# Performance work log

Hardware: AMD Instinct MI355X
Metric: run time of the kernel (lower is better)

## Reference

```python
import jax, jax.numpy as jnp
import numpy as np
from jax import lax

C = 64          # in_c
D_INNER = 128   # expand=2 * C
D_STATE = 16
D_CONV = 4
DT_RANK = 4     # ceil(C/16)
B, H, W = 4, 64, 64


def setup_inputs() -> dict:
    key = jax.random.key(0)
    ks = jax.random.split(key, 22)
    def n(k, shape, s=0.05):
        return jax.random.normal(k, shape, jnp.float32) * s
    inp = {}
    inp["x"] = jax.random.normal(ks[0], (B, C, H, W), jnp.float32)
    # AxialDW: depthwise (3,1) and (1,3) convs, groups=C
    inp["dwh_w"] = n(ks[1], (C, 1, 3, 1), 0.2); inp["dwh_b"] = n(ks[2], (C,))
    inp["dww_w"] = n(ks[3], (C, 1, 1, 3), 0.2); inp["dww_b"] = n(ks[4], (C,))
    # 1x1 conv
    inp["conv_w"] = n(ks[5], (C, C, 1, 1), 0.1); inp["conv_b"] = n(ks[6], (C,))
    # BatchNorm (eval mode, running stats)
    inp["bn_g"] = jnp.ones((C,), jnp.float32); inp["bn_b"] = jnp.zeros((C,), jnp.float32)
    inp["bn_m"] = n(ks[7], (C,), 0.1)
    inp["bn_v"] = jnp.abs(n(ks[8], (C,), 0.1)) + 1.0
    # ResMambaBlock: LayerNorm + Mamba(d_model=C) + residual
    inp["ln_g"] = jnp.ones((C,), jnp.float32); inp["ln_b"] = jnp.zeros((C,), jnp.float32)
    inp["in_proj_w"] = n(ks[9], (2 * D_INNER, C))
    inp["convd_w"] = n(ks[10], (D_INNER, 1, D_CONV), 0.2); inp["convd_b"] = n(ks[11], (D_INNER,))
    inp["x_proj_w"] = n(ks[12], (DT_RANK + 2 * D_STATE, D_INNER))
    inp["dt_proj_w"] = n(ks[13], (D_INNER, DT_RANK), 0.2)
    inp["dt_proj_b"] = n(ks[14], (D_INNER,), 0.5) - 4.0  # softplus -> small dt
    inp["A_log"] = jnp.log(jnp.tile(jnp.arange(1, D_STATE + 1, dtype=jnp.float32), (D_INNER, 1)))
    inp["Dp"] = jnp.ones((D_INNER,), jnp.float32)
    inp["out_proj_w"] = n(ks[15], (C, D_INNER))
    return inp


def _mamba(h, in_proj_w, convd_w, convd_b, x_proj_w, dt_proj_w, dt_proj_b, A_log, Dp, out_proj_w):
    # h: [B, L, C]
    Bt, L, _ = h.shape
    xz = jnp.einsum('blc,dc->bld', h, in_proj_w)          # [B,L,2*D_INNER]
    xm, z = jnp.split(xz, 2, axis=-1)
    # causal depthwise conv1d over L
    xc = lax.conv_general_dilated(xm.transpose(0, 2, 1), convd_w, (1,), [(D_CONV - 1, 0)],
                                  feature_group_count=D_INNER,
                                  dimension_numbers=('NCH', 'OIH', 'NCH'))
    xc = jax.nn.silu(xc + convd_b[None, :, None]).transpose(0, 2, 1)  # [B,L,D_INNER]
    dbc = jnp.einsum('bld,ed->ble', xc, x_proj_w)
    dt, Bm, Cm = jnp.split(dbc, [DT_RANK, DT_RANK + D_STATE], axis=-1)
    dt = jax.nn.softplus(jnp.einsum('blr,dr->bld', dt, dt_proj_w) + dt_proj_b)  # [B,L,D_INNER]
    A = -jnp.exp(A_log)                                    # [D_INNER, D_STATE]
    dA = jnp.exp(dt[..., None] * A)                        # [B,L,D_INNER,D_STATE]
    dBx = dt[..., None] * Bm[:, :, None, :] * xc[..., None]  # [B,L,D_INNER,D_STATE]

    def step(hc, inp):
        dA_t, dBx_t, C_t = inp
        hc = hc * dA_t + dBx_t                             # [B,D_INNER,D_STATE]
        y = jnp.einsum('bds,bs->bd', hc, C_t)
        return hc, y

    h0 = jnp.zeros((Bt, D_INNER, D_STATE), h.dtype)
    _, ys = lax.scan(step, h0, (dA.transpose(1, 0, 2, 3), dBx.transpose(1, 0, 2, 3), Cm.transpose(1, 0, 2)))
    ys = ys.transpose(1, 0, 2)                             # [B,L,D_INNER]
    ys = (ys + xc * Dp) * jax.nn.silu(z)
    return jnp.einsum('bld,cd->blc', ys, out_proj_w)


def _forward(x, dwh_w, dwh_b, dww_w, dww_b, conv_w, conv_b, bn_g, bn_b, bn_m, bn_v,
             ln_g, ln_b, in_proj_w, convd_w, convd_b, x_proj_w, dt_proj_w, dt_proj_b,
             A_log, Dp, out_proj_w):
    dn = ('NCHW', 'OIHW', 'NCHW')
    xh = lax.conv_general_dilated(x, dwh_w, (1, 1), 'SAME', feature_group_count=C, dimension_numbers=dn)
    xw = lax.conv_general_dilated(x, dww_w, (1, 1), 'SAME', feature_group_count=C, dimension_numbers=dn)
    x = x + xh + dwh_b[None, :, None, None] + xw + dww_b[None, :, None, None]
    x = lax.conv_general_dilated(x, conv_w, (1, 1), 'SAME', dimension_numbers=dn) + conv_b[None, :, None, None]
    x = (x - bn_m[None, :, None, None]) * lax.rsqrt(bn_v + 1e-5)[None, :, None, None] \
        * bn_g[None, :, None, None] + bn_b[None, :, None, None]
    x = jax.nn.relu(x)
    # ResMambaBlock: LN + Mamba + residual over tokens [B, H*W, C]
    Bt, Cc, Hh, Ww = x.shape
    seq = x.reshape(Bt, Cc, Hh * Ww).transpose(0, 2, 1)    # [B,L,C]
    mu = seq.mean(-1, keepdims=True)
    var = ((seq - mu) ** 2).mean(-1, keepdims=True)
    hn = (seq - mu) * lax.rsqrt(var + 1e-5) * ln_g + ln_b
    y = _mamba(hn, in_proj_w, convd_w, convd_b, x_proj_w, dt_proj_w, dt_proj_b, A_log, Dp, out_proj_w)
    out = (y + seq).transpose(0, 2, 1).reshape(Bt, Cc, Hh, Ww)
    return out


def reference(x, dwh_w, dwh_b, dww_w, dww_b, conv_w, conv_b, bn_g, bn_b, bn_m, bn_v,
              ln_g, ln_b, in_proj_w, convd_w, convd_b, x_proj_w, dt_proj_w, dt_proj_b,
              A_log, Dp, out_proj_w):
    return _forward(x, dwh_w, dwh_b, dww_w, dww_b, conv_w, conv_b, bn_g, bn_b, bn_m, bn_v,
                    ln_g, ln_b, in_proj_w, convd_w, convd_b, x_proj_w, dt_proj_w, dt_proj_b,
                    A_log, Dp, out_proj_w)
```

## Files before the change

### kernel.cpp

```cpp
#include <hip/hip_runtime.h>
#include <hip/hip_bf16.h>
#include <math.h>

#define BB 4
#define CC 64
#define LL 4096
#define DI 128
#define DS 16
#define NC 64
#define CL 64

__global__ __launch_bounds__(256) void k12_front(
    const float* __restrict__ x, const float* __restrict__ dwh_w,
    const float* __restrict__ dwh_b, const float* __restrict__ dww_w,
    const float* __restrict__ dww_b, const float* __restrict__ conv_w,
    const float* __restrict__ conv_b, const float* __restrict__ bn_g,
    const float* __restrict__ bn_b, const float* __restrict__ bn_m,
    const float* __restrict__ bn_v, const float* __restrict__ ln_g,
    const float* __restrict__ ln_b, float* __restrict__ seqT,
    float* __restrict__ hn) {
  __shared__ __align__(16) float tsm[64 * 68];
  __shared__ __align__(16) float wt[64 * 68];
  __shared__ float vsm[64 * 65];
  int tid = threadIdx.x;
  int blk = blockIdx.x;
  int b = blk >> 6, h = blk & 63;
  for (int i = tid; i < 4096; i += 256) {
    int co = i >> 6, ci = i & 63;
    wt[ci * 68 + co] = conv_w[i];
  }
  for (int i = tid; i < 4096; i += 256) {
    int c = i >> 6, w = i & 63;
    int base = ((b * 64 + c) << 12) + (h << 6) + w;
    float cen = x[base];
    float up = (h > 0)  ? x[base - 64] : 0.f;
    float dn = (h < 63) ? x[base + 64] : 0.f;
    float lf = (w > 0)  ? x[base - 1]  : 0.f;
    float rt = (w < 63) ? x[base + 1]  : 0.f;
    float t = cen + dwh_w[c*3]*up + dwh_w[c*3+1]*cen + dwh_w[c*3+2]*dn + dwh_b[c]
                  + dww_w[c*3]*lf + dww_w[c*3+1]*cen + dww_w[c*3+2]*rt + dww_b[c];
    tsm[c * 68 + w] = t;
  }
  __syncthreads();
  int co0 = (tid & 15) << 2;
  int w0  = (tid >> 4) << 2;
  float acc[4][4] = {};
  #pragma unroll 8
  for (int ci = 0; ci < 64; ++ci) {
    const float4 w4 = *(const float4*)&wt[ci * 68 + co0];
    const float4 t4 = *(const float4*)&tsm[ci * 68 + w0];
    const float wv[4] = {w4.x, w4.y, w4.z, w4.w};
    const float tv[4] = {t4.x, t4.y, t4.z, t4.w};
    #pragma unroll
    for (int jc = 0; jc < 4; ++jc)
      #pragma unroll
      for (int iw = 0; iw < 4; ++iw)
        acc[jc][iw] = fmaf(wv[jc], tv[iw], acc[jc][iw]);
  }
  #pragma unroll
  for (int j = 0; j < 4; ++j) {
    int co = co0 + j;
    float sc = bn_g[co] * rsqrtf(bn_v[co] + 1e-5f);
    float sh = bn_b[co] - bn_m[co] * sc;
    float cb = conv_b[co];
    float4 o4;
    float* oo = (float*)&o4;
    #pragma unroll
    for (int i = 0; i < 4; ++i) {
      float v = fmaxf(fmaf(acc[j][i] + cb, sc, sh), 0.f);
      vsm[(w0 + i) * 65 + co] = v;
      oo[i] = v;
    }
    *(float4*)&seqT[((size_t)(b * 64 + co) << 12) + (h << 6) + w0] = o4;
  }
  __syncthreads();
  int lane = tid & 63, wv_ = tid >> 6;
  float lg = ln_g[lane], lb = ln_b[lane];
  for (int k = 0; k < 16; ++k) {
    int w = wv_ * 16 + k;
    float v = vsm[w * 65 + lane];
    float sum = v, sq = v * v;
    #pragma unroll
    for (int off = 1; off < 64; off <<= 1) {
      sum += __shfl_xor(sum, off, 64);
      sq  += __shfl_xor(sq,  off, 64);
    }
    float mu  = sum * (1.f / 64.f);
    float var = sq * (1.f / 64.f) - mu * mu;
    float inv = rsqrtf(var + 1e-5f);
    hn[((size_t)((b << 12) + (h << 6) + w) << 6) + lane] = (v - mu) * inv * lg + lb;
  }
}

__global__ __launch_bounds__(256) void k3_inproj(
    const float* __restrict__ hn, const float* __restrict__ ipw,
    float* __restrict__ xm, float* __restrict__ z) {
  __shared__ __align__(16) float wsm[64 * 132];
  __shared__ __align__(16) float hsm[64 * 68];
  int tid = threadIdx.x;
  int half = blockIdx.y;
  int blk = blockIdx.x;
  int b  = blk >> 6;
  int l0 = (blk & 63) << 6;
  const float* wsrc = ipw + half * 8192;
  for (int i = tid; i < 8192; i += 256) {
    int d = i >> 6, c = i & 63;
    wsm[c * 132 + d] = wsrc[i];
  }
  for (int i = tid; i < 4096; i += 256) {
    int t = i >> 6, c = i & 63;
    hsm[c * 68 + t] = hn[((size_t)(b * LL + l0) << 6) + i];
  }
  __syncthreads();
  int d0 = (tid & 31) << 2;
  int t0 = (tid >> 5) << 3;
  float acc[4][8] = {};
  #pragma unroll 8
  for (int c = 0; c < 64; ++c) {
    const float4 w4 = *(const float4*)&wsm[c * 132 + d0];
    const float4 h0 = *(const float4*)&hsm[c * 68 + t0];
    const float4 h1 = *(const float4*)&hsm[c * 68 + t0 + 4];
    const float wv[4] = {w4.x, w4.y, w4.z, w4.w};
    const float hv[8] = {h0.x, h0.y, h0.z, h0.w, h1.x, h1.y, h1.z, h1.w};
    #pragma unroll
    for (int i = 0; i < 4; ++i)
      #pragma unroll
      for (int j = 0; j < 8; ++j)
        acc[i][j] = fmaf(wv[i], hv[j], acc[i][j]);
  }
  float* dst = half ? z : xm;
  #pragma unroll
  for (int j = 0; j < 8; ++j) {
    float4 v = make_float4(acc[0][j], acc[1][j], acc[2][j], acc[3][j]);
    *(float4*)&dst[((size_t)(b * LL + l0 + t0 + j) << 7) + d0] = v;
  }
}

__global__ __launch_bounds__(128) void k4_conv_proj(
    const float* __restrict__ xm, const float* __restrict__ convd_w,
    const float* __restrict__ convd_b, const float* __restrict__ xpw,
    const float* __restrict__ dpw, const float* __restrict__ dpb,
    float* __restrict__ xc_g, float* __restrict__ dt_g,
    float* __restrict__ Bm_g, float* __restrict__ Cm_g) {
  __shared__ float xms[11 * 128];
  __shared__ __align__(16) float xcs[8 * 132];
  __shared__ __align__(16) float xpwt[36 * 132];
  __shared__ __align__(16) float dbcs[8 * 36];
  int tid = threadIdx.x;
  int blk = blockIdx.x;
  int b  = blk >> 9;
  int l0 = (blk & 511) << 3;
  for (int r = 0; r < 11; ++r) {
    int l = l0 - 3 + r;
    xms[r * 128 + tid] = (l >= 0) ? xm[((size_t)(b * LL + l) << 7) + tid] : 0.f;
  }
  for (int i = tid; i < 4608; i += 128) {
    int e = i >> 7, d = i & 127;
    xpwt[e * 132 + d] = xpw[i];
  }
  __syncthreads();
  float4 cw = *(const float4*)&convd_w[tid * 4];
  float cb = convd_b[tid];
  #pragma unroll
  for (int t = 0; t < 8; ++t) {
    float pre = cb + cw.x * xms[t*128 + tid] + cw.y * xms[(t+1)*128 + tid]
                   + cw.z * xms[(t+2)*128 + tid] + cw.w * xms[(t+3)*128 + tid];
    float v = pre / (1.f + __expf(-pre));
    xcs[t * 132 + tid] = v;
    xc_g[((size_t)(b * LL + l0 + t) << 7) + tid] = v;
  }
  __syncthreads();
  for (int pp = tid; pp < 288; pp += 128) {
    int t = pp / 36, e = pp - t * 36;
    float acc = 0.f;
    #pragma unroll 8
    for (int d0 = 0; d0 < 128; d0 += 4) {
      const float4 a = *(const float4*)&xcs[t * 132 + d0];
      const float4 w = *(const float4*)&xpwt[e * 132 + d0];
      acc = fmaf(a.x, w.x, acc); acc = fmaf(a.y, w.y, acc);
      acc = fmaf(a.z, w.z, acc); acc = fmaf(a.w, w.w, acc);
    }
    dbcs[t * 36 + e] = acc;
  }
  __syncthreads();
  float4 dw = *(const float4*)&dpw[tid * 4];
  float bb = dpb[tid];
  #pragma unroll
  for (int t = 0; t < 8; ++t) {
    const float4 dd = *(const float4*)&dbcs[t * 36];
    float raw = bb + dw.x * dd.x + dw.y * dd.y + dw.z * dd.z + dw.w * dd.w;
    float sp = (raw > 20.f) ? raw : log1pf(__expf(raw));
    dt_g[((size_t)(b * LL + l0 + t) << 7) + tid] = sp;
  }
  int tl = tid >> 4, s = tid & 15;
  Bm_g[((size_t)(b * LL + l0 + tl) << 4) + s] = dbcs[tl * 36 + 4 + s];
  Cm_g[((size_t)(b * LL + l0 + tl) << 4) + s] = dbcs[tl * 36 + 20 + s];
}

__global__ __launch_bounds__(256) void k5a_chunk(
    const float* __restrict__ dt_g, const float* __restrict__ Bm_g,
    const float* __restrict__ xc_g, const float* __restrict__ A_log,
    float* __restrict__ h_end, float* __restrict__ Pp) {
  int blk = blockIdx.x;
  int b = blk >> 6, ch = blk & 63;
  int tid = threadIdx.x;
  int d = tid & 127, s0 = (tid >> 7) << 3;
  int l0 = ch << 6;
  const float* dt_p = dt_g + ((size_t)b << 19);
  const float* xc_p = xc_g + ((size_t)b << 19);
  const float* Bm_p = Bm_g + ((size_t)b << 16);
  float A[8], h[8], p[8];
  #pragma unroll
  for (int q = 0; q < 2; ++q) {
    float4 a4 = *(const float4*)&A_log[d * 16 + s0 + q * 4];
    A[q*4]   = -__expf(a4.x); A[q*4+1] = -__expf(a4.y);
    A[q*4+2] = -__expf(a4.z); A[q*4+3] = -__expf(a4.w);
  }
  #pragma unroll
  for (int s = 0; s < 8; ++s) { h[s] = 0.f; p[s] = 1.f; }
  #pragma unroll 2
  for (int i = 0; i < CL; ++i) {
    int l = l0 + i;
    float dtv = dt_p[(l << 7) + d];
    float xcv = xc_p[(l << 7) + d];
    float dtx = dtv * xcv;
    float Bv[8];
    #pragma unroll
    for (int q = 0; q < 2; ++q) {
      float4 b4 = *(const float4*)&Bm_p[(l << 4) + s0 + q * 4];
      Bv[q*4] = b4.x; Bv[q*4+1] = b4.y; Bv[q*4+2] = b4.z; Bv[q*4+3] = b4.w;
    }
    #pragma unroll
    for (int s = 0; s < 8; ++s) {
      float dA = __expf(dtv * A[s]);
      h[s] = fmaf(h[s], dA, dtx * Bv[s]);
      p[s] *= dA;
    }
  }
  float* he = h_end + ((((size_t)blk << 7) + d) << 4) + s0;
  float* pe = Pp    + ((((size_t)blk << 7) + d) << 4) + s0;
  #pragma unroll
  for (int q = 0; q < 2; ++q) {
    *(float4*)&he[q * 4] = make_float4(h[q*4], h[q*4+1], h[q*4+2], h[q*4+3]);
    *(float4*)&pe[q * 4] = make_float4(p[q*4], p[q*4+1], p[q*4+2], p[q*4+3]);
  }
}

__global__ __launch_bounds__(128) void k5b_carry(
    const float* __restrict__ h_end, const float* __restrict__ Pp,
    float* __restrict__ h_in) {
  int g = blockIdx.x * 128 + threadIdx.x;
  int b = g >> 11;
  int r = g & 2047;
  size_t o = ((size_t)b << 17) + r;
  float H = 0.f;
  #pragma unroll 4
  for (int c = 0; c < NC; ++c) {
    size_t oc = o + ((size_t)c << 11);
    h_in[oc] = H;
    H = fmaf(H, Pp[oc], h_end[oc]);
  }
}

__global__ __launch_bounds__(256) void k56_scan_out(
    const float* __restrict__ dt_g, const float* __restrict__ Bm_g,
    const float* __restrict__ Cm_g, const float* __restrict__ xc_g,
    const float* __restrict__ A_log, const float* __restrict__ h_in,
    const float* __restrict__ z_g, const float* __restrict__ Dp,
    const float* __restrict__ opw, const float* __restrict__ seqT,
    float* __restrict__ out) {
  __shared__ __align__(16) float ysm[128 * 64];
  __shared__ __align__(16) float wsm[128 * 64];
  int tid = threadIdx.x;
  int blk = blockIdx.x;
  int b = blk >> 6, ch = blk & 63;
  int l0 = ch << 6;
  if (tid < 128) {
    int d = tid;
    const float* dt_p = dt_g + ((size_t)b << 19);
    const float* xc_p = xc_g + ((size_t)b << 19);
    const float* z_p  = z_g  + ((size_t)b << 19);
    const float* Bm_p = Bm_g + ((size_t)b << 16);
    const float* Cm_p = Cm_g + ((size_t)b << 16);
    float A[16], h[16];
    const float* hi = h_in + ((((size_t)blk << 7) + d) << 4);
    #pragma unroll
    for (int q = 0; q < 4; ++q) {
      float4 a4 = *(const float4*)&A_log[d * 16 + q * 4];
      A[q*4]   = -__expf(a4.x); A[q*4+1] = -__expf(a4.y);
      A[q*4+2] = -__expf(a4.z); A[q*4+3] = -__expf(a4.w);
      float4 h4 = *(const float4*)&hi[q * 4];
      h[q*4] = h4.x; h[q*4+1] = h4.y; h[q*4+2] = h4.z; h[q*4+3] = h4.w;
    }
    float dpv = Dp[d];
    int sw = (d & 15) << 2;
    #pragma unroll 2
    for (int i = 0; i < CL; ++i) {
      int l = l0 + i;
      float dtv = dt_p[(l << 7) + d];
      float xcv = xc_p[(l << 7) + d];
      float dtx = dtv * xcv;
      float Bv[16], Cv[16];
      #pragma unroll
      for (int q4 = 0; q4 < 4; ++q4) {
        float4 b4 = *(const float4*)&Bm_p[(l << 4) + q4 * 4];
        float4 c4 = *(const float4*)&Cm_p[(l << 4) + q4 * 4];
        Bv[q4*4] = b4.x; Bv[q4*4+1] = b4.y; Bv[q4*4+2] = b4.z; Bv[q4*4+3] = b4.w;
        Cv[q4*4] = c4.x; Cv[q4*4+1] = c4.y; Cv[q4*4+2] = c4.z; Cv[q4*4+3] = c4.w;
      }
      float y = 0.f;
      #pragma unroll
      for (int s = 0; s < 16; ++s) {
        float dA = __expf(dtv * A[s]);
        h[s] = fmaf(h[s], dA, dtx * Bv[s]);
        y = fmaf(h[s], Cv[s], y);
      }
      float zz = z_p[(l << 7) + d];
      float sil = zz / (1.f + __expf(-zz));
      ysm[(d << 6) + ((i + sw) & 63)] = (y + xcv * dpv) * sil;
    }
  } else {
    for (int i = tid - 128; i < 8192; i += 128) {
      int cc = i >> 7, d = i & 127;
      wsm[(d << 6) + ((cc + ((d & 15) << 2)) & 63)] = opw[i];
    }
  }
  __syncthreads();
  int t0 = (tid >> 4) << 2;
  int c0 = (tid & 15) << 2;
  float acc[4][4] = {};
  #pragma unroll 4
  for (int d = 0; d < 128; ++d) {
    int sw = (d & 15) << 2;
    const float4 y4 = *(const float4*)&ysm[(d << 6) + ((t0 + sw) & 63)];
    const float4 w4 = *(const float4*)&wsm[(d << 6) + ((c0 + sw) & 63)];
    const float yv[4] = {y4.x, y4.y, y4.z, y4.w};
    const float wv[4] = {w4.x, w4.y, w4.z, w4.w};
    #pragma unroll
    for (int i = 0; i < 4; ++i)
      #pragma unroll
      for (int j = 0; j < 4; ++j)
        acc[i][j] = fmaf(yv[i], wv[j], acc[i][j]);
  }
  #pragma unroll
  for (int j = 0; j < 4; ++j) {
    size_t row = ((size_t)(b * 64 + c0 + j) << 12) + l0 + t0;
    float4 s4 = *(const float4*)&seqT[row];
    float4 o4 = make_float4(acc[0][j] + s4.x, acc[1][j] + s4.y,
                            acc[2][j] + s4.z, acc[3][j] + s4.w);
    *(float4*)&out[row] = o4;
  }
}

extern "C" void kernel_launch(void* const* d_in, const int* in_sizes, int n_in,
                              void* d_out, int out_size, void* d_ws, size_t ws_size,
                              hipStream_t stream) {
  const float* x       = (const float*)d_in[0];
  const float* dwh_w   = (const float*)d_in[1];
  const float* dwh_b   = (const float*)d_in[2];
  const float* dww_w   = (const float*)d_in[3];
  const float* dww_b   = (const float*)d_in[4];
  const float* conv_w  = (const float*)d_in[5];
  const float* conv_b  = (const float*)d_in[6];
  const float* bn_g    = (const float*)d_in[7];
  const float* bn_b    = (const float*)d_in[8];
  const float* bn_m    = (const float*)d_in[9];
  const float* bn_v    = (const float*)d_in[10];
  const float* ln_g    = (const float*)d_in[11];
  const float* ln_b    = (const float*)d_in[12];
  const float* ipw     = (const float*)d_in[13];
  const float* convd_w = (const float*)d_in[14];
  const float* convd_b = (const float*)d_in[15];
  const float* xpw     = (const float*)d_in[16];
  const float* dpw     = (const float*)d_in[17];
  const float* dpb     = (const float*)d_in[18];
  const float* A_log   = (const float*)d_in[19];
  const float* Dp      = (const float*)d_in[20];
  const float* opw     = (const float*)d_in[21];
  float* out = (float*)d_out;

  float* ws = (float*)d_ws;
  const size_t M = 1048576;
  const size_t K = 262144;
  float* seqT  = ws + 0;
  float* hn    = ws + M;
  float* h_end = ws + M;
  float* P_buf = ws + M + 2 * K;
  float* Bm    = ws + 2 * M;
  float* Cm    = ws + 2 * M + K;
  float* h_in  = ws + 2 * M + 2 * K;
  float* xm    = ws + 3 * M;
  float* z_buf = ws + 5 * M;
  float* xc    = ws + 7 * M;
  float* dt    = ws + 9 * M;

  k12_front<<<256, 256, 0, stream>>>(x, dwh_w, dwh_b, dww_w, dww_b, conv_w,
                                     conv_b, bn_g, bn_b, bn_m, bn_v, ln_g,
                                     ln_b, seqT, hn);
  k3_inproj<<<dim3(256, 2), 256, 0, stream>>>(hn, ipw, xm, z_buf);
  k4_conv_proj<<<2048, 128, 0, stream>>>(xm, convd_w, convd_b, xpw, dpw, dpb,
                                         xc, dt, Bm, Cm);
  k5a_chunk<<<BB * NC, 256, 0, stream>>>(dt, Bm, xc, A_log, h_end, P_buf);
  k5b_carry<<<64, 128, 0, stream>>>(h_end, P_buf, h_in);
  k56_scan_out<<<BB * NC, 256, 0, stream>>>(dt, Bm, Cm, xc, A_log, h_in,
                                            z_buf, Dp, opw, seqT, out);
}
```

Measured before the change: 210.6 us.

## Fuse chunked scan stages into cooperative kernel and split front kernel by width halves

Merges the three scan kernels (chunk-local scan, carry propagation, scan+output projection) into one cooperative kernel with grid-wide syncs, removing two kernel launches and their boundaries. The front kernel now uses 512 blocks, each covering half of a row's width, to raise parallelism, and writes seqT through a shared-memory transpose for coalescing. The cost is grid.sync overhead and a requirement that all 256 blocks are co-resident. The carry step now runs on only 32 of the 256 blocks while the rest wait at the barrier.

```diff
diff --git a/kernel.cpp b/kernel.cpp
--- a/kernel.cpp
+++ b/kernel.cpp
@@ -1,6 +1,9 @@
 #include <hip/hip_runtime.h>
 #include <hip/hip_bf16.h>
+#include <hip/hip_cooperative_groups.h>
 #include <math.h>
+
+namespace cg = cooperative_groups;
 
 #define BB 4
 #define CC 64
@@ -19,76 +22,79 @@
     const float* __restrict__ bn_v, const float* __restrict__ ln_g,
     const float* __restrict__ ln_b, float* __restrict__ seqT,
     float* __restrict__ hn) {
-  __shared__ __align__(16) float tsm[64 * 68];
+  __shared__ __align__(16) float tsm[64 * 36];
   __shared__ __align__(16) float wt[64 * 68];
-  __shared__ float vsm[64 * 65];
+  __shared__ float vsm[32 * 65];
   int tid = threadIdx.x;
   int blk = blockIdx.x;
-  int b = blk >> 6, h = blk & 63;
+  int b = blk >> 7, h = (blk >> 1) & 63, wh = blk & 1;
+  int wbase = wh << 5;
   for (int i = tid; i < 4096; i += 256) {
     int co = i >> 6, ci = i & 63;
     wt[ci * 68 + co] = conv_w[i];
   }
-  for (int i = tid; i < 4096; i += 256) {
-    int c = i >> 6, w = i & 63;
+  for (int i = tid; i < 2048; i += 256) {
+    int c = i >> 5, wl = i & 31;
+    int w = wbase + wl;
     int base = ((b * 64 + c) << 12) + (h << 6) + w;
     float cen = x[base];
     float up = (h > 0)  ? x[base - 64] : 0.f;
     float dn = (h < 63) ? x[base + 64] : 0.f;
     float lf = (w > 0)  ? x[base - 1]  : 0.f;
     float rt = (w < 63) ? x[base + 1]  : 0.f;
-    float t = cen + dwh_w[c*3]*up + dwh_w[c*3+1]*cen + dwh_w[c*3+2]*dn + dwh_b[c]
-                  + dww_w[c*3]*lf + dww_w[c*3+1]*cen + dww_w[c*3+2]*rt + dww_b[c];
-    tsm[c * 68 + w] = t;
-  }
-  __syncthreads();
-  int co0 = (tid & 15) << 2;
-  int w0  = (tid >> 4) << 2;
-  float acc[4][4] = {};
-  #pragma unroll 8
-  for (int ci = 0; ci < 64; ++ci) {
-    const float4 w4 = *(const float4*)&wt[ci * 68 + co0];
-    const float4 t4 = *(const float4*)&tsm[ci * 68 + w0];
-    const float wv[4] = {w4.x, w4.y, w4.z, w4.w};
-    const float tv[4] = {t4.x, t4.y, t4.z, t4.w};
-    #pragma unroll
-    for (int jc = 0; jc < 4; ++jc)
-      #pragma unroll
-      for (int iw = 0; iw < 4; ++iw)
-        acc[jc][iw] = fmaf(wv[jc], tv[iw], acc[jc][iw]);
-  }
-  #pragma unroll
-  for (int j = 0; j < 4; ++j) {
-    int co = co0 + j;
-    float sc = bn_g[co] * rsqrtf(bn_v[co] + 1e-5f);
-    float sh = bn_b[co] - bn_m[co] * sc;
-    float cb = conv_b[co];
-    float4 o4;
-    float* oo = (float*)&o4;
-    #pragma unroll
-    for (int i = 0; i < 4; ++i) {
-      float v = fmaxf(fmaf(acc[j][i] + cb, sc, sh), 0.f);
-      vsm[(w0 + i) * 65 + co] = v;
-      oo[i] = v;
-    }
-    *(float4*)&seqT[((size_t)(b * 64 + co) << 12) + (h << 6) + w0] = o4;
-  }
-  __syncthreads();
-  int lane = tid & 63, wv_ = tid >> 6;
-  float lg = ln_g[lane], lb = ln_b[lane];
-  for (int k = 0; k < 16; ++k) {
-    int w = wv_ * 16 + k;
-    float v = vsm[w * 65 + lane];
-    float sum = v, sq = v * v;
-    #pragma unroll
-    for (int off = 1; off < 64; off <<= 1) {
-      sum += __shfl_xor(sum, off, 64);
-      sq  += __shfl_xor(sq,  off, 64);
-    }
-    float mu  = sum * (1.f / 64.f);
-    float var = sq * (1.f / 64.f) - mu * mu;
-    float inv = rsqrtf(var + 1e-5f);
-    hn[((size_t)((b << 12) + (h << 6) + w) << 6) + lane] = (v - mu) * inv * lg + lb;
+    tsm[c * 36 + wl] =
+        cen + dwh_w[c*3]*up + dwh_w[c*3+1]*cen + dwh_w[c*3+2]*dn + dwh_b[c]
+            + dww_w[c*3]*lf + dww_w[c*3+1]*cen + dww_w[c*3+2]*rt + dww_b[c];
+  }
+  __syncthreads();
+  {
+    int co0 = (tid & 15) << 2;
+    int wl0 = (tid >> 4) << 1;
+    float acc[4][2] = {};
+    #pragma unroll 8
+    for (int ci = 0; ci < 64; ++ci) {
+      const float4 w4 = *(const float4*)&wt[ci * 68 + co0];
+      const float2 t2 = *(const float2*)&tsm[ci * 36 + wl0];
+      const float wv[4] = {w4.x, w4.y, w4.z, w4.w};
+      #pragma unroll
+      for (int jc = 0; jc < 4; ++jc) {
+        acc[jc][0] = fmaf(wv[jc], t2.x, acc[jc][0]);
+        acc[jc][1] = fmaf(wv[jc], t2.y, acc[jc][1]);
+      }
+    }
+    #pragma unroll
+    for (int j = 0; j < 4; ++j) {
+      int co = co0 + j;
+      float sc = bn_g[co] * rsqrtf(bn_v[co] + 1e-5f);
+      float sh = bn_b[co] - bn_m[co] * sc;
+      float cb = conv_b[co];
+      vsm[wl0 * 65 + co]       = fmaxf(fmaf(acc[j][0] + cb, sc, sh), 0.f);
+      vsm[(wl0 + 1) * 65 + co] = fmaxf(fmaf(acc[j][1] + cb, sc, sh), 0.f);
+    }
+  }
+  __syncthreads();
+  for (int i = tid; i < 2048; i += 256) {
+    int co = i >> 5, wl = i & 31;
+    seqT[((size_t)(b * 64 + co) << 12) + (h << 6) + wbase + wl] = vsm[wl * 65 + co];
+  }
+  {
+    int lane = tid & 63, wv_ = tid >> 6;
+    float lg = ln_g[lane], lb = ln_b[lane];
+    for (int k = 0; k < 8; ++k) {
+      int wl = wv_ * 8 + k;
+      float v = vsm[wl * 65 + lane];
+      float sum = v, sq = v * v;
+      #pragma unroll
+      for (int off = 1; off < 64; off <<= 1) {
+        sum += __shfl_xor(sum, off, 64);
+        sq  += __shfl_xor(sq,  off, 64);
+      }
+      float mu  = sum * (1.f / 64.f);
+      float var = sq * (1.f / 64.f) - mu * mu;
+      float inv = rsqrtf(var + 1e-5f);
+      hn[((size_t)((b << 12) + (h << 6) + wbase + wl) << 6) + lane] =
+          (v - mu) * inv * lg + lb;
+    }
   }
 }
 
@@ -197,84 +203,81 @@
   Cm_g[((size_t)(b * LL + l0 + tl) << 4) + s] = dbcs[tl * 36 + 20 + s];
 }
 
-__global__ __launch_bounds__(256) void k5a_chunk(
-    const float* __restrict__ dt_g, const float* __restrict__ Bm_g,
-    const float* __restrict__ xc_g, const float* __restrict__ A_log,
-    float* __restrict__ h_end, float* __restrict__ Pp) {
-  int blk = blockIdx.x;
-  int b = blk >> 6, ch = blk & 63;
-  int tid = threadIdx.x;
-  int d = tid & 127, s0 = (tid >> 7) << 3;
-  int l0 = ch << 6;
-  const float* dt_p = dt_g + ((size_t)b << 19);
-  const float* xc_p = xc_g + ((size_t)b << 19);
-  const float* Bm_p = Bm_g + ((size_t)b << 16);
-  float A[8], h[8], p[8];
-  #pragma unroll
-  for (int q = 0; q < 2; ++q) {
-    float4 a4 = *(const float4*)&A_log[d * 16 + s0 + q * 4];
-    A[q*4]   = -__expf(a4.x); A[q*4+1] = -__expf(a4.y);
-    A[q*4+2] = -__expf(a4.z); A[q*4+3] = -__expf(a4.w);
-  }
-  #pragma unroll
-  for (int s = 0; s < 8; ++s) { h[s] = 0.f; p[s] = 1.f; }
-  #pragma unroll 2
-  for (int i = 0; i < CL; ++i) {
-    int l = l0 + i;
-    float dtv = dt_p[(l << 7) + d];
-    float xcv = xc_p[(l << 7) + d];
-    float dtx = dtv * xcv;
-    float Bv[8];
-    #pragma unroll
-    for (int q = 0; q < 2; ++q) {
-      float4 b4 = *(const float4*)&Bm_p[(l << 4) + s0 + q * 4];
-      Bv[q*4] = b4.x; Bv[q*4+1] = b4.y; Bv[q*4+2] = b4.z; Bv[q*4+3] = b4.w;
-    }
-    #pragma unroll
-    for (int s = 0; s < 8; ++s) {
-      float dA = __expf(dtv * A[s]);
-      h[s] = fmaf(h[s], dA, dtx * Bv[s]);
-      p[s] *= dA;
-    }
-  }
-  float* he = h_end + ((((size_t)blk << 7) + d) << 4) + s0;
-  float* pe = Pp    + ((((size_t)blk << 7) + d) << 4) + s0;
-  #pragma unroll
-  for (int q = 0; q < 2; ++q) {
-    *(float4*)&he[q * 4] = make_float4(h[q*4], h[q*4+1], h[q*4+2], h[q*4+3]);
-    *(float4*)&pe[q * 4] = make_float4(p[q*4], p[q*4+1], p[q*4+2], p[q*4+3]);
-  }
-}
-
-__global__ __launch_bounds__(128) void k5b_carry(
-    const float* __restrict__ h_end, const float* __restrict__ Pp,
-    float* __restrict__ h_in) {
-  int g = blockIdx.x * 128 + threadIdx.x;
-  int b = g >> 11;
-  int r = g & 2047;
-  size_t o = ((size_t)b << 17) + r;
-  float H = 0.f;
-  #pragma unroll 4
-  for (int c = 0; c < NC; ++c) {
-    size_t oc = o + ((size_t)c << 11);
-    h_in[oc] = H;
-    H = fmaf(H, Pp[oc], h_end[oc]);
-  }
-}
-
-__global__ __launch_bounds__(256) void k56_scan_out(
+__global__ __launch_bounds__(256) void k5_coop(
     const float* __restrict__ dt_g, const float* __restrict__ Bm_g,
     const float* __restrict__ Cm_g, const float* __restrict__ xc_g,
-    const float* __restrict__ A_log, const float* __restrict__ h_in,
+    const float* __restrict__ A_log, float* __restrict__ h_end,
+    float* __restrict__ Pp, float* __restrict__ h_in,
     const float* __restrict__ z_g, const float* __restrict__ Dp,
     const float* __restrict__ opw, const float* __restrict__ seqT,
     float* __restrict__ out) {
   __shared__ __align__(16) float ysm[128 * 64];
   __shared__ __align__(16) float wsm[128 * 64];
+  cg::grid_group grid = cg::this_grid();
   int tid = threadIdx.x;
   int blk = blockIdx.x;
   int b = blk >> 6, ch = blk & 63;
   int l0 = ch << 6;
+  {
+    int d = tid & 127, s0 = (tid >> 7) << 3;
+    const float* dt_p = dt_g + ((size_t)b << 19);
+    const float* xc_p = xc_g + ((size_t)b << 19);
+    const float* Bm_p = Bm_g + ((size_t)b << 16);
+    float A[8], h[8], p[8];
+    #pragma unroll
+    for (int q = 0; q < 2; ++q) {
+      float4 a4 = *(const float4*)&A_log[d * 16 + s0 + q * 4];
+      A[q*4]   = -__expf(a4.x); A[q*4+1] = -__expf(a4.y);
+      A[q*4+2] = -__expf(a4.z); A[q*4+3] = -__expf(a4.w);
+    }
+    #pragma unroll
+    for (int s = 0; s < 8; ++s) { h[s] = 0.f; p[s] = 1.f; }
+    #pragma unroll 2
+    for (int i = 0; i < CL; ++i) {
+      int l = l0 + i;
+      float dtv = dt_p[(l << 7) + d];
+      float xcv = xc_p[(l << 7) + d];
+      float dtx = dtv * xcv;
+      float Bv[8];
+      #pragma unroll
+      for (int q = 0; q < 2; ++q) {
+        float4 b4 = *(const float4*)&Bm_p[(l << 4) + s0 + q * 4];
+        Bv[q*4] = b4.x; Bv[q*4+1] = b4.y; Bv[q*4+2] = b4.z; Bv[q*4+3] = b4.w;
+      }
+      #pragma unroll
+      for (int s = 0; s < 8; ++s) {
+        float dA = __expf(dtv * A[s]);
+        h[s] = fmaf(h[s], dA, dtx * Bv[s]);
+        p[s] *= dA;
+      }
+    }
+    float* he = h_end + ((((size_t)blk << 7) + d) << 4) + s0;
+    float* pe = Pp    + ((((size_t)blk << 7) + d) << 4) + s0;
+    #pragma unroll
+    for (int q = 0; q < 2; ++q) {
+      *(float4*)&he[q * 4] = make_float4(h[q*4], h[q*4+1], h[q*4+2], h[q*4+3]);
+      *(float4*)&pe[q * 4] = make_float4(p[q*4], p[q*4+1], p[q*4+2], p[q*4+3]);
+    }
+  }
+  __threadfence();
+  grid.sync();
+  {
+    int g = blk * 256 + tid;
+    if (g < 8192) {
+      int bb_ = g >> 11;
+      int r = g & 2047;
+      size_t o = ((size_t)bb_ << 17) + r;
+      float H = 0.f;
+      #pragma unroll 4
+      for (int c = 0; c < NC; ++c) {
+        size_t oc = o + ((size_t)c << 11);
+        h_in[oc] = H;
+        H = fmaf(H, Pp[oc], h_end[oc]);
+      }
+    }
+  }
+  __threadfence();
+  grid.sync();
   if (tid < 128) {
     int d = tid;
     const float* dt_p = dt_g + ((size_t)b << 19);
@@ -394,14 +397,19 @@
   float* xc    = ws + 7 * M;
   float* dt    = ws + 9 * M;
 
-  k12_front<<<256, 256, 0, stream>>>(x, dwh_w, dwh_b, dww_w, dww_b, conv_w,
+  k12_front<<<512, 256, 0, stream>>>(x, dwh_w, dwh_b, dww_w, dww_b, conv_w,
                                      conv_b, bn_g, bn_b, bn_m, bn_v, ln_g,
                                      ln_b, seqT, hn);
   k3_inproj<<<dim3(256, 2), 256, 0, stream>>>(hn, ipw, xm, z_buf);
   k4_conv_proj<<<2048, 128, 0, stream>>>(xm, convd_w, convd_b, xpw, dpw, dpb,
                                          xc, dt, Bm, Cm);
-  k5a_chunk<<<BB * NC, 256, 0, stream>>>(dt, Bm, xc, A_log, h_end, P_buf);
-  k5b_carry<<<64, 128, 0, stream>>>(h_end, P_buf, h_in);
-  k56_scan_out<<<BB * NC, 256, 0, stream>>>(dt, Bm, Cm, xc, A_log, h_in,
-                                            z_buf, Dp, opw, seqT, out);
+  {
+    void* args[] = {
+      (void*)&dt, (void*)&Bm, (void*)&Cm, (void*)&xc, (void*)&A_log,
+      (void*)&h_end, (void*)&P_buf, (void*)&h_in, (void*)&z_buf,
+      (void*)&Dp, (void*)&opw, (void*)&seqT, (void*)&out
+    };
+    hipLaunchCooperativeKernel((void*)k5_coop, dim3(BB * NC), dim3(256),
+                               args, 0, stream);
+  }
 }
```

Result: slower. 353.8 us (+68.0%).

## Halve scan chunk length so all threads run the selective scan

Applied to the files above, without the earlier changes.

The chunked selective scan now uses 128 chunks of 32 steps instead of 64 of 64. In the scan/out-projection kernel both halves of the block each scan one sub-chunk, where before half the block only loaded weights. The serial critical path per block is halved, at the cost of a longer carry pass and larger h_end/P buffers, which are moved in the workspace. The exponentials also switch to exp2f with log2e folded into A.

```diff
diff --git a/kernel.cpp b/kernel.cpp
--- a/kernel.cpp
+++ b/kernel.cpp
@@ -7,8 +7,9 @@
 #define LL 4096
 #define DI 128
 #define DS 16
-#define NC 64
-#define CL 64
+#define NC 128
+#define CL 32
+#define LOG2E 1.4426950408889634f
 
 __global__ __launch_bounds__(256) void k12_front(
     const float* __restrict__ x, const float* __restrict__ dwh_w,
@@ -202,10 +203,10 @@
     const float* __restrict__ xc_g, const float* __restrict__ A_log,
     float* __restrict__ h_end, float* __restrict__ Pp) {
   int blk = blockIdx.x;
-  int b = blk >> 6, ch = blk & 63;
+  int b = blk >> 7, ch = blk & (NC - 1);
   int tid = threadIdx.x;
   int d = tid & 127, s0 = (tid >> 7) << 3;
-  int l0 = ch << 6;
+  int l0 = ch << 5;
   const float* dt_p = dt_g + ((size_t)b << 19);
   const float* xc_p = xc_g + ((size_t)b << 19);
   const float* Bm_p = Bm_g + ((size_t)b << 16);
@@ -213,8 +214,8 @@
   #pragma unroll
   for (int q = 0; q < 2; ++q) {
     float4 a4 = *(const float4*)&A_log[d * 16 + s0 + q * 4];
-    A[q*4]   = -__expf(a4.x); A[q*4+1] = -__expf(a4.y);
-    A[q*4+2] = -__expf(a4.z); A[q*4+3] = -__expf(a4.w);
+    A[q*4]   = -__expf(a4.x) * LOG2E; A[q*4+1] = -__expf(a4.y) * LOG2E;
+    A[q*4+2] = -__expf(a4.z) * LOG2E; A[q*4+3] = -__expf(a4.w) * LOG2E;
   }
   #pragma unroll
   for (int s = 0; s < 8; ++s) { h[s] = 0.f; p[s] = 1.f; }
@@ -232,7 +233,7 @@
     }
     #pragma unroll
     for (int s = 0; s < 8; ++s) {
-      float dA = __expf(dtv * A[s]);
+      float dA = exp2f(dtv * A[s]);
       h[s] = fmaf(h[s], dA, dtx * Bv[s]);
       p[s] *= dA;
     }
@@ -246,13 +247,13 @@
   }
 }
 
-__global__ __launch_bounds__(128) void k5b_carry(
+__global__ __launch_bounds__(256) void k5b_carry(
     const float* __restrict__ h_end, const float* __restrict__ Pp,
     float* __restrict__ h_in) {
-  int g = blockIdx.x * 128 + threadIdx.x;
+  int g = blockIdx.x * 256 + threadIdx.x;
   int b = g >> 11;
   int r = g & 2047;
-  size_t o = ((size_t)b << 17) + r;
+  size_t o = ((size_t)b << 18) + r;
   float H = 0.f;
   #pragma unroll 4
   for (int c = 0; c < NC; ++c) {
@@ -275,28 +276,36 @@
   int blk = blockIdx.x;
   int b = blk >> 6, ch = blk & 63;
   int l0 = ch << 6;
-  if (tid < 128) {
-    int d = tid;
+  for (int i = tid; i < 8192; i += 256) {
+    int cc = i >> 7, d = i & 127;
+    wsm[(d << 6) + ((cc + ((d & 15) << 2)) & 63)] = opw[i];
+  }
+  {
+    int q = tid >> 7;
+    int d = tid & 127;
+    int cidx = (ch << 1) + q;
+    int lc0 = cidx << 5;
     const float* dt_p = dt_g + ((size_t)b << 19);
     const float* xc_p = xc_g + ((size_t)b << 19);
     const float* z_p  = z_g  + ((size_t)b << 19);
     const float* Bm_p = Bm_g + ((size_t)b << 16);
     const float* Cm_p = Cm_g + ((size_t)b << 16);
     float A[16], h[16];
-    const float* hi = h_in + ((((size_t)blk << 7) + d) << 4);
-    #pragma unroll
-    for (int q = 0; q < 4; ++q) {
-      float4 a4 = *(const float4*)&A_log[d * 16 + q * 4];
-      A[q*4]   = -__expf(a4.x); A[q*4+1] = -__expf(a4.y);
-      A[q*4+2] = -__expf(a4.z); A[q*4+3] = -__expf(a4.w);
-      float4 h4 = *(const float4*)&hi[q * 4];
-      h[q*4] = h4.x; h[q*4+1] = h4.y; h[q*4+2] = h4.z; h[q*4+3] = h4.w;
+    const float* hi = h_in + ((size_t)b << 18) + ((size_t)cidx << 11) + (d << 4);
+    #pragma unroll
+    for (int q4 = 0; q4 < 4; ++q4) {
+      float4 a4 = *(const float4*)&A_log[d * 16 + q4 * 4];
+      A[q4*4]   = -__expf(a4.x) * LOG2E; A[q4*4+1] = -__expf(a4.y) * LOG2E;
+      A[q4*4+2] = -__expf(a4.z) * LOG2E; A[q4*4+3] = -__expf(a4.w) * LOG2E;
+      float4 h4 = *(const float4*)&hi[q4 * 4];
+      h[q4*4] = h4.x; h[q4*4+1] = h4.y; h[q4*4+2] = h4.z; h[q4*4+3] = h4.w;
     }
     float dpv = Dp[d];
     int sw = (d & 15) << 2;
+    int t_off = q << 5;
     #pragma unroll 2
     for (int i = 0; i < CL; ++i) {
-      int l = l0 + i;
+      int l = lc0 + i;
       float dtv = dt_p[(l << 7) + d];
       float xcv = xc_p[(l << 7) + d];
       float dtx = dtv * xcv;
@@ -311,18 +320,13 @@
       float y = 0.f;
       #pragma unroll
       for (int s = 0; s < 16; ++s) {
-        float dA = __expf(dtv * A[s]);
+        float dA = exp2f(dtv * A[s]);
         h[s] = fmaf(h[s], dA, dtx * Bv[s]);
         y = fmaf(h[s], Cv[s], y);
       }
       float zz = z_p[(l << 7) + d];
       float sil = zz / (1.f + __expf(-zz));
-      ysm[(d << 6) + ((i + sw) & 63)] = (y + xcv * dpv) * sil;
-    }
-  } else {
-    for (int i = tid - 128; i < 8192; i += 128) {
-      int cc = i >> 7, d = i & 127;
-      wsm[(d << 6) + ((cc + ((d & 15) << 2)) & 63)] = opw[i];
+      ysm[(d << 6) + ((t_off + i + sw) & 63)] = (y + xcv * dpv) * sil;
     }
   }
   __syncthreads();
@@ -384,12 +388,12 @@
   const size_t K = 262144;
   float* seqT  = ws + 0;
   float* hn    = ws + M;
-  float* h_end = ws + M;
-  float* P_buf = ws + M + 2 * K;
+  float* h_in  = ws + M;
   float* Bm    = ws + 2 * M;
   float* Cm    = ws + 2 * M + K;
-  float* h_in  = ws + 2 * M + 2 * K;
   float* xm    = ws + 3 * M;
+  float* h_end = ws + 3 * M;
+  float* P_buf = ws + 4 * M;
   float* z_buf = ws + 5 * M;
   float* xc    = ws + 7 * M;
   float* dt    = ws + 9 * M;
@@ -401,7 +405,7 @@
   k4_conv_proj<<<2048, 128, 0, stream>>>(xm, convd_w, convd_b, xpw, dpw, dpb,
                                          xc, dt, Bm, Cm);
   k5a_chunk<<<BB * NC, 256, 0, stream>>>(dt, Bm, xc, A_log, h_end, P_buf);
-  k5b_carry<<<64, 128, 0, stream>>>(h_end, P_buf, h_in);
-  k56_scan_out<<<BB * NC, 256, 0, stream>>>(dt, Bm, Cm, xc, A_log, h_in,
+  k5b_carry<<<32, 256, 0, stream>>>(h_end, P_buf, h_in);
+  k56_scan_out<<<BB * 64, 256, 0, stream>>>(dt, Bm, Cm, xc, A_log, h_in,
                                             z_buf, Dp, opw, seqT, out);
 }
```

New measurement: 220.3 us. +4.6%, slower.
